# Kernel optimization log

Measured on AMD Instinct MI355X. Metric: run time of the kernel, lower is better.

Reference implementation:

```python
import jax, jax.numpy as jnp
import numpy as np

N_HEAD = 12

def setup_inputs() -> dict:
    key = jax.random.key(0)
    ks = jax.random.split(key, 5)
    C = 768
    B, T = 2, 2048
    s = 0.02
    x = jax.random.normal(ks[0], (B, T, C), dtype=jnp.float32)
    W_attn = jax.random.normal(ks[1], (C, 3 * C), dtype=jnp.float32) * s
    b_attn = jnp.zeros((3 * C,), dtype=jnp.float32)
    W_proj = jax.random.normal(ks[2], (C, C), dtype=jnp.float32) * s
    b_proj = jnp.zeros((C,), dtype=jnp.float32)
    return {"x": x, "W_attn": W_attn, "b_attn": b_attn, "W_proj": W_proj, "b_proj": b_proj}

def reference(x, W_attn, b_attn, W_proj, b_proj):
    B, T, C = x.shape
    H = N_HEAD
    hs = C // H
    qkv = x @ W_attn + b_attn                      # [B,T,3C]
    q, k, v = jnp.split(qkv, 3, axis=2)
    # [B,H,T,hs]
    q = q.reshape(B, T, H, hs).transpose(0, 2, 1, 3)
    k = k.reshape(B, T, H, hs).transpose(0, 2, 1, 3)
    v = v.reshape(B, T, H, hs).transpose(0, 2, 1, 3)
    scale = 1.0 / np.sqrt(hs).astype(np.float32)
    att = jnp.einsum('bhqd,bhkd->bhqk', q, k) * scale   # [B,H,T,T]
    causal = jnp.tril(jnp.ones((T, T), dtype=bool))
    att = jnp.where(causal, att, -jnp.inf)
    att = jax.nn.softmax(att, axis=-1)
    y = jnp.einsum('bhqk,bhkd->bhqd', att, v)            # [B,H,T,hs]
    y = y.transpose(0, 2, 1, 3).reshape(B, T, C)
    return y @ W_proj + b_proj
```

## Files before the change

### kernel.cpp

```cpp
#include <hip/hip_runtime.h>


#define BB 2
#define TT 2048
#define CC 768
#define C3 2304
#define HH 12
#define DD 64
#define MM 4096

typedef unsigned short u16;
typedef unsigned int u32;
typedef __attribute__((ext_vector_type(8))) u16 u16x8;
typedef __attribute__((ext_vector_type(8))) __bf16 bf16x8;
typedef __attribute__((ext_vector_type(4))) float f32x4;
typedef __attribute__((ext_vector_type(16))) float f32x16;

__device__ __forceinline__ float u2f(u16 u) {
    union { u32 i; float f; } c; c.i = ((u32)u) << 16; return c.f;
}
__device__ __forceinline__ u16 f2u(float f) {
    union { float f; u32 i; } c; c.f = f;
    u32 x = c.i;
    return (u16)((x + 0x7FFFu + ((x >> 16) & 1u)) >> 16);
}
__device__ __forceinline__ u16 f2b(float f) {
    __bf16 h = (__bf16)f; return __builtin_bit_cast(u16, h);
}
__device__ __forceinline__ bf16x8 ldsb8(const u16* p) {
    return __builtin_bit_cast(bf16x8, *(const u16x8*)p);
}
__device__ __forceinline__ f32x4 mfma16(bf16x8 a, bf16x8 b, f32x4 c) {
    return __builtin_amdgcn_mfma_f32_16x16x32_bf16(a, b, c, 0, 0, 0);
}
__device__ __forceinline__ f32x16 mfma32(bf16x8 a, bf16x8 b, f32x16 c) {
    return __builtin_amdgcn_mfma_f32_32x32x16_bf16(a, b, c, 0, 0, 0);
}
typedef __attribute__((address_space(1))) const u32 gu32;
typedef __attribute__((address_space(3))) u32 lu32;
__device__ __forceinline__ void gload16(const u16* gp, u16* lp) {
    __builtin_amdgcn_global_load_lds((gu32*)(const void*)gp, (lu32*)(void*)lp,
                                     16, 0, 0);
}
__device__ __forceinline__ void barrier_raw() {
    asm volatile("" ::: "memory");
    __builtin_amdgcn_s_barrier();
    asm volatile("" ::: "memory");
}

__global__ void detect_kernel(const u16* __restrict__ x, int* __restrict__ flag)
{
    __shared__ int found;
    if (threadIdx.x == 0) found = 0;
    __syncthreads();
    int local = 0;
    const u16x8* p = (const u16x8*)x + threadIdx.x;
    #pragma unroll
    for (int i = 0; i < 8; ++i) {
        const u16x8 v = p[(size_t)i * 256];
        #pragma unroll
        for (int j = 0; j < 8; ++j)
            if ((v[j] & 0x7F80u) == 0x7F80u) local = 1;
    }
    if (local) atomicOr(&found, 1);
    __syncthreads();
    if (threadIdx.x == 0) *flag = found ? 1 : 0;
}

__device__ void prep_w_body(const void* __restrict__ Wv, u16* __restrict__ Wt,
                            int K, int N, int bx, int by, int fm,
                            u16 (*Ts)[72])
{
    const int t = threadIdx.x;
    const int n0 = bx * 64, k0 = by * 64;
    const int r = t >> 2, c0 = (t & 3) << 4;

    if (fm) {
        const float* W = (const float*)Wv + (size_t)(k0 + r) * N + n0 + c0;
        #pragma unroll
        for (int i = 0; i < 16; i += 4) {
            const float4 v = *(const float4*)(W + i);
            Ts[c0 + i + 0][r] = f2u(v.x);
            Ts[c0 + i + 1][r] = f2u(v.y);
            Ts[c0 + i + 2][r] = f2u(v.z);
            Ts[c0 + i + 3][r] = f2u(v.w);
        }
    } else {
        const u16* W = (const u16*)Wv + (size_t)(k0 + r) * N + n0 + c0;
        const u16x8 a = *(const u16x8*)W;
        const u16x8 c = *(const u16x8*)(W + 8);
        #pragma unroll
        for (int i = 0; i < 8; ++i) { Ts[c0 + i][r] = a[i]; Ts[c0 + 8 + i][r] = c[i]; }
    }
    __syncthreads();
    u16* o = Wt + (size_t)(n0 + r) * K + k0 + c0;
    *(u16x8*)o = *(const u16x8*)&Ts[r][c0];
    *(u16x8*)(o + 8) = *(const u16x8*)&Ts[r][c0 + 8];
}

__global__ __launch_bounds__(256)
void fused_prep(const void* __restrict__ x, const void* __restrict__ Wa,
                const void* __restrict__ ba, const void* __restrict__ Wp,
                const void* __restrict__ bp,
                u16* __restrict__ xb, u16* __restrict__ WaT,
                u16* __restrict__ WpT, u16* __restrict__ bao,
                u16* __restrict__ bpo,
                const int* __restrict__ flag, int mode)
{
    __shared__ u16 Ts[64][72];
    const int fm = (mode >= 0) ? mode : *flag;
    const int blk = blockIdx.x;
    const int t = threadIdx.x;

    if (blk < 432) {
        prep_w_body(Wa, WaT, CC, C3, blk % 36, blk / 36, fm, Ts);
    } else if (blk < 576) {
        const int b2 = blk - 432;
        prep_w_body(Wp, WpT, CC, CC, b2 % 12, b2 / 12, fm, Ts);
    } else if (blk < 2112) {
        if (fm == 0) return;
        const size_t i = (size_t)(blk - 576) * 256 + t;
        const float* xp = (const float*)x + i * 8;
        u16x8 o;
        #pragma unroll
        for (int j = 0; j < 8; ++j) o[j] = f2u(xp[j]);
        *(u16x8*)(xb + i * 8) = o;
    } else {
        const int i = (blk - 2112) * 256 + t;
        if (i < C3) bao[i] = fm ? f2u(((const float*)ba)[i]) : ((const u16*)ba)[i];
        if (i < CC) bpo[i] = fm ? f2u(((const float*)bp)[i]) : ((const u16*)bp)[i];
    }
}

template <int FRM, int FRN>
__global__ __launch_bounds__(256)
void gemm_mfma(const u16* __restrict__ Adir, const u16* __restrict__ Acnv,
               const u16* __restrict__ Bt, const u16* __restrict__ bias,
               void* __restrict__ outv, int M, int N, int K,
               const int* __restrict__ flag, int mode, int om_sel)
{
    constexpr int TSM = 32 * FRM, TSN = 32 * FRN;
    constexpr int LPA = TSM / 64;
    constexpr int LPB = TSN / 64;

    __shared__ u16 As[2][TSM * 32];
    __shared__ u16 Bs[2][TSN * 32];

    const int fm = (mode >= 0) ? mode : *flag;
    const u16* A = fm ? Acnv : Adir;
    const int om = om_sel ? fm : 0;

    const int nwg = gridDim.x;
    const int lin = (blockIdx.x & 7) * (nwg >> 3) + (blockIdx.x >> 3);
    const int nx = N / TSN;
    const int m0 = (lin / nx) * TSM, n0 = (lin % nx) * TSN;

    const int t = threadIdx.x;
    const int lane = t & 63, wave = t >> 6;
    const int wm = wave >> 1, wn = wave & 1;
    const int l15 = lane & 15, h4 = lane >> 4;

    const int rsub = lane >> 2;
    const int cs = ((lane & 3) ^ ((lane >> 4) & 3)) * 8;
    const u16* Ab[LPA];
    const u16* Bb[LPB];
    #pragma unroll
    for (int j = 0; j < LPA; ++j)
        Ab[j] = A + (size_t)(m0 + wave * (16 * LPA) + j * 16 + rsub) * K + cs;
    #pragma unroll
    for (int j = 0; j < LPB; ++j)
        Bb[j] = Bt + (size_t)(n0 + wave * (16 * LPB) + j * 16 + rsub) * K + cs;

    f32x4 acc[FRM][FRN];
    #pragma unroll
    for (int i = 0; i < FRM; ++i)
        #pragma unroll
        for (int j = 0; j < FRN; ++j) acc[i][j] = (f32x4){0.f, 0.f, 0.f, 0.f};

    const int csr = (h4 ^ (l15 >> 2)) * 8;
    const int arow = wm * (TSM / 2) + l15;
    const int brow = wn * (TSN / 2) + l15;

    const int NT = K >> 5;
    #pragma unroll
    for (int j = 0; j < LPA; ++j)
        gload16(Ab[j], &As[0][(wave * LPA + j) * 512]);
    #pragma unroll
    for (int j = 0; j < LPB; ++j)
        gload16(Bb[j], &Bs[0][(wave * LPB + j) * 512]);

    for (int kt = 0; kt < NT; ++kt) {
        const int cur = kt & 1;
        if (kt + 1 < NT) {
            const int k0 = (kt + 1) << 5;
            const int nb = cur ^ 1;
            #pragma unroll
            for (int j = 0; j < LPA; ++j)
                gload16(Ab[j] + k0, &As[nb][(wave * LPA + j) * 512]);
            #pragma unroll
            for (int j = 0; j < LPB; ++j)
                gload16(Bb[j] + k0, &Bs[nb][(wave * LPB + j) * 512]);
            if constexpr (LPA + LPB == 4)
                asm volatile("s_waitcnt vmcnt(4)" ::: "memory");
            else if constexpr (LPA + LPB == 3)
                asm volatile("s_waitcnt vmcnt(3)" ::: "memory");
            else
                asm volatile("s_waitcnt vmcnt(2)" ::: "memory");
        } else {
            asm volatile("s_waitcnt vmcnt(0)" ::: "memory");
        }
        barrier_raw();

        bf16x8 af[FRM], bfr[FRN];
        #pragma unroll
        for (int f = 0; f < FRM; ++f)
            af[f] = ldsb8(&As[cur][(arow + f * 16) * 32 + csr]);
        #pragma unroll
        for (int f = 0; f < FRN; ++f)
            bfr[f] = ldsb8(&Bs[cur][(brow + f * 16) * 32 + csr]);
        #pragma unroll
        for (int i = 0; i < FRM; ++i)
            #pragma unroll
            for (int j = 0; j < FRN; ++j)
                acc[i][j] = mfma16(af[i], bfr[j], acc[i][j]);

        barrier_raw();
    }

    const int orow = m0 + wm * (TSM / 2) + h4 * 4;
    const int ocol = n0 + wn * (TSN / 2) + l15;
    if (om == 0) {
        u16* out = (u16*)outv;
        #pragma unroll
        for (int i = 0; i < FRM; ++i)
            #pragma unroll
            for (int j = 0; j < FRN; ++j) {
                const int col = ocol + j * 16;
                const float bv = u2f(bias[col]);
                #pragma unroll
                for (int r2 = 0; r2 < 4; ++r2)
                    out[(size_t)(orow + i * 16 + r2) * N + col] = f2b(acc[i][j][r2] + bv);
            }
    } else {
        float* out = (float*)outv;
        #pragma unroll
        for (int i = 0; i < FRM; ++i)
            #pragma unroll
            for (int j = 0; j < FRN; ++j) {
                const int col = ocol + j * 16;
                const float bv = u2f(bias[col]);
                #pragma unroll
                for (int r2 = 0; r2 < 4; ++r2)
                    out[(size_t)(orow + i * 16 + r2) * N + col] = acc[i][j][r2] + bv;
            }
    }
}

__global__ __launch_bounds__(256)
void attn_mfma(const u16* __restrict__ qkv, u16* __restrict__ yatt)
{
    __shared__ u16 Ks[2][64][72];
    __shared__ u16 Vt[2][64][72];

    const int bid = blockIdx.x;
    const int bin = bid & 255, slot = bid >> 8;
    const int g = bin >> 5, j = bin & 31;
    int qt;
    if (slot == 0)      qt = j;
    else if (slot == 1) qt = (j + 16) & 31;
    else                qt = (j < 16) ? (30 - 2 * j) : (63 - 2 * j);
    const int hb = slot * 8 + g;
    const int h = hb % HH, b = hb / HH;

    const int t = threadIdx.x;
    const int lane = t & 63, w = t >> 6;
    const int l31 = lane & 31, hl = lane >> 5;
    const int qh = w >> 1, kh = w & 1;
    const int q0 = qt * 64;
    const int qg = q0 + qh * 32 + l31;

    const int sr = t >> 2;
    const int sd = (t & 3) << 4;
    const int k5 = sr & 31;
    const int rr = (sr & 32) | (((k5 >> 2) & 1) << 4) | (((k5 >> 4) & 1) << 3)
                 | (((k5 >> 3) & 1) << 2) | (k5 & 3);
    const int vk = (t & 31) * 2;
    const int vd = (t >> 5) << 3;

    bf16x8 qf[4];
    {
        const u16* qp = qkv + ((size_t)(b * TT + qg)) * C3 + h * DD + hl * 8;
        #pragma unroll
        for (int t4 = 0; t4 < 4; ++t4) {
            const u16x8 v = *(const u16x8*)(qp + 16 * t4);
            #pragma unroll
            for (int i = 0; i < 8; ++i)
                qf[t4][i] = (__bf16)(u2f(v[i]) * 0.125f);
        }
    }

    float m_i = -1e4f, l_p = 0.f;
    f32x16 O0, O1;
    #pragma unroll
    for (int i = 0; i < 16; ++i) { O0[i] = 0.f; O1[i] = 0.f; }

    const u16* kB = qkv + ((size_t)(b * TT + sr)) * C3 + CC + h * DD + sd;
    const u16* vB = qkv + ((size_t)(b * TT + vk)) * C3 + 2 * CC + h * DD + vd;

    const int NT = qt + 1;

    u16x8 kr0 = *(const u16x8*)kB;
    u16x8 kr1 = *(const u16x8*)(kB + 8);
    u16x8 vr0 = *(const u16x8*)vB;
    u16x8 vr1 = *(const u16x8*)(vB + C3);
    *(u16x8*)&Ks[0][rr][sd]     = kr0;
    *(u16x8*)&Ks[0][rr][sd + 8] = kr1;
    #pragma unroll
    for (int i = 0; i < 8; ++i)
        *(u32*)&Vt[0][vd + i][vk] = (u32)vr0[i] | ((u32)vr1[i] << 16);
    if (NT > 1) {
        const u16* kp = kB + (size_t)64 * C3;
        const u16* vp = vB + (size_t)64 * C3;
        kr0 = *(const u16x8*)kp;
        kr1 = *(const u16x8*)(kp + 8);
        vr0 = *(const u16x8*)vp;
        vr1 = *(const u16x8*)(vp + C3);
    }
    __syncthreads();

    for (int kt = 0; kt < NT; ++kt) {
        const int cur = kt & 1;

        f32x16 s;
        #pragma unroll
        for (int i = 0; i < 16; ++i) s[i] = 0.f;
        __builtin_amdgcn_s_setprio(1);
        #pragma unroll
        for (int t4 = 0; t4 < 4; ++t4)
            s = mfma32(ldsb8(&Ks[cur][kh * 32 + l31][t4 * 16 + hl * 8]),
                       qf[t4], s);
        __builtin_amdgcn_s_setprio(0);

        if (kt + 1 < NT) {
            const int nb = cur ^ 1;
            *(u16x8*)&Ks[nb][rr][sd]     = kr0;
            *(u16x8*)&Ks[nb][rr][sd + 8] = kr1;
            #pragma unroll
            for (int i = 0; i < 8; ++i)
                *(u32*)&Vt[nb][vd + i][vk] = (u32)vr0[i] | ((u32)vr1[i] << 16);
            if (kt + 2 < NT) {
                const u16* kp = kB + (size_t)(kt + 2) * 64 * C3;
                const u16* vp = vB + (size_t)(kt + 2) * 64 * C3;
                kr0 = *(const u16x8*)kp;
                kr1 = *(const u16x8*)(kp + 8);
                vr0 = *(const u16x8*)vp;
                vr1 = *(const u16x8*)(vp + C3);
            }
        }

        if (kt == qt) {
            #pragma unroll
            for (int jj = 0; jj < 4; ++jj)
                #pragma unroll
                for (int e = 0; e < 4; ++e) {
                    const int kl = kh * 32 + ((jj & 1) << 4) + (hl << 3)
                                 + ((jj >> 1) << 2) + e;
                    if (kt * 64 + kl > qg) s[4 * jj + e] = -1e30f;
                }
        }

        float pm = s[0];
        #pragma unroll
        for (int i = 1; i < 16; ++i) pm = fmaxf(pm, s[i]);

        if (!__all(pm <= m_i + 8.f)) {
            const float pr = fmaxf(pm, __shfl_xor(pm, 32));
            const float mnew = fmaxf(m_i, pr);
            const float a_ = __expf(m_i - mnew);
            l_p *= a_;
            #pragma unroll
            for (int i = 0; i < 16; ++i) { O0[i] *= a_; O1[i] *= a_; }
            m_i = mnew;
        }

        bf16x8 p0, p1;
        float rs = 0.f;
        #pragma unroll
        for (int e = 0; e < 4; ++e) {
            const float a = __expf(s[e] - m_i);       rs += a; p0[e]     = (__bf16)a;
            const float c = __expf(s[8 + e] - m_i);   rs += c; p0[4 + e] = (__bf16)c;
            const float d = __expf(s[4 + e] - m_i);   rs += d; p1[e]     = (__bf16)d;
            const float g2 = __expf(s[12 + e] - m_i); rs += g2; p1[4 + e] = (__bf16)g2;
        }
        l_p += rs;

        __builtin_amdgcn_s_setprio(1);
        O0 = mfma32(ldsb8(&Vt[cur][l31][kh * 32 + hl * 8]), p0, O0);
        O0 = mfma32(ldsb8(&Vt[cur][l31][kh * 32 + 16 + hl * 8]), p1, O0);
        O1 = mfma32(ldsb8(&Vt[cur][32 + l31][kh * 32 + hl * 8]), p0, O1);
        O1 = mfma32(ldsb8(&Vt[cur][32 + l31][kh * 32 + 16 + hl * 8]), p1, O1);
        __builtin_amdgcn_s_setprio(0);

        __syncthreads();
    }

    const float lr = l_p + __shfl_xor(l_p, 32);

    float* scr = (float*)&Ks[0][0][0];
    const int sidx = (qh * 64 + lane) * 34;
    if (kh == 1) {
        scr[sidx] = m_i;
        scr[sidx + 1] = lr;
        #pragma unroll
        for (int i = 0; i < 16; ++i) {
            scr[sidx + 2 + i] = O0[i];
            scr[sidx + 18 + i] = O1[i];
        }
    }
    __syncthreads();
    if (kh == 0) {
        const float mB = scr[sidx], lB = scr[sidx + 1];
        const float mm = fmaxf(m_i, mB);
        const float a0 = __expf(m_i - mm), a1 = __expf(mB - mm);
        const float inv = 1.0f / (lr * a0 + lB * a1);
        u16* yp = yatt + ((size_t)(b * TT + qg)) * CC + h * DD;
        #pragma unroll
        for (int r = 0; r < 16; ++r) {
            const int drow = (r & 3) + 8 * (r >> 2) + 4 * hl;
            yp[drow]      = f2b((O0[r] * a0 + scr[sidx + 2 + r] * a1) * inv);
            yp[32 + drow] = f2b((O1[r] * a0 + scr[sidx + 18 + r] * a1) * inv);
        }
    }
}

extern "C" void kernel_launch(void* const* d_in, const int* in_sizes, int n_in,
                              void* d_out, int out_size, void* d_ws, size_t ws_size,
                              hipStream_t stream)
{
    (void)n_in; (void)out_size; (void)ws_size;

    const void* x      = d_in[0];
    const void* W_attn = d_in[1];
    const void* b_attn = d_in[2];
    const void* W_proj = d_in[3];
    const void* b_proj = d_in[4];

    u16* qkv  = (u16*)d_ws;
    u16* yatt = qkv + (size_t)MM * C3;
    u16* xb   = yatt;
    u16* WaT  = yatt + (size_t)MM * CC;
    u16* WpT  = WaT + (size_t)C3 * CC;
    u16* ba   = WpT + (size_t)CC * CC;
    u16* bp   = ba + C3;
    int* flag = (int*)(bp + CC);

    int mode = -1;
    if (in_sizes[0] == MM * CC * 4) mode = 1;
    else if (in_sizes[0] == MM * CC * 2) mode = 0;
    if (mode < 0) {
        detect_kernel<<<1, 256, 0, stream>>>((const u16*)x, flag);
    }

    fused_prep<<<2121, 256, 0, stream>>>(x, W_attn, b_attn, W_proj, b_proj,
                                         xb, WaT, WpT, ba, bp, flag, mode);

    gemm_mfma<4, 2><<<(MM / 128) * (C3 / 64), 256, 0, stream>>>(
        (const u16*)x, xb, WaT, ba, (void*)qkv, MM, C3, CC, flag, mode, 0);

    attn_mfma<<<dim3(TT / 64 * HH * BB, 1, 1), 256, 0, stream>>>(qkv, yatt);

    gemm_mfma<2, 2><<<(MM / 64) * (CC / 64), 256, 0, stream>>>(
        yatt, yatt, WpT, bp, d_out, MM, CC, CC, flag, mode, 1);
}
```

Baseline: 169.1 us.

## Use persistent attention blocks with atomic work queue, longest-first ordering

Replaces the static block-to-query-tile mapping in the attention kernel with persistent blocks that fetch work items from a global atomic counter. Items are ordered longest causal tile first, so the uneven causal workload is balanced dynamically across CUs. The counter is reset inside the prep kernel. Each item now costs an atomic plus an extra barrier, and 1024 blocks are launched for 768 items, so some blocks exit without doing any work.

```diff
diff --git a/kernel.cpp b/kernel.cpp
--- a/kernel.cpp
+++ b/kernel.cpp
@@ -8,6 +8,7 @@
 #define HH 12
 #define DD 64
 #define MM 4096
+#define NITEMS (32 * HH * BB)
 
 typedef unsigned short u16;
 typedef unsigned int u32;
@@ -105,7 +106,7 @@
                 u16* __restrict__ xb, u16* __restrict__ WaT,
                 u16* __restrict__ WpT, u16* __restrict__ bao,
                 u16* __restrict__ bpo,
-                const int* __restrict__ flag, int mode)
+                const int* __restrict__ flag, int mode, int* __restrict__ qcnt)
 {
     __shared__ u16 Ts[64][72];
     const int fm = (mode >= 0) ? mode : *flag;
@@ -126,6 +127,7 @@
         for (int j = 0; j < 8; ++j) o[j] = f2u(xp[j]);
         *(u16x8*)(xb + i * 8) = o;
     } else {
+        if (blk == 2112 && t == 0) *qcnt = 0;
         const int i = (blk - 2112) * 256 + t;
         if (i < C3) bao[i] = fm ? f2u(((const float*)ba)[i]) : ((const u16*)ba)[i];
         if (i < CC) bpo[i] = fm ? f2u(((const float*)bp)[i]) : ((const u16*)bp)[i];
@@ -257,27 +259,17 @@
 }
 
 __global__ __launch_bounds__(256)
-void attn_mfma(const u16* __restrict__ qkv, u16* __restrict__ yatt)
+void attn_mfma(const u16* __restrict__ qkv, u16* __restrict__ yatt,
+               int* __restrict__ qcnt)
 {
     __shared__ u16 Ks[2][64][72];
     __shared__ u16 Vt[2][64][72];
-
-    const int bid = blockIdx.x;
-    const int bin = bid & 255, slot = bid >> 8;
-    const int g = bin >> 5, j = bin & 31;
-    int qt;
-    if (slot == 0)      qt = j;
-    else if (slot == 1) qt = (j + 16) & 31;
-    else                qt = (j < 16) ? (30 - 2 * j) : (63 - 2 * j);
-    const int hb = slot * 8 + g;
-    const int h = hb % HH, b = hb / HH;
+    __shared__ int s_item;
 
     const int t = threadIdx.x;
     const int lane = t & 63, w = t >> 6;
     const int l31 = lane & 31, hl = lane >> 5;
     const int qh = w >> 1, kh = w & 1;
-    const int q0 = qt * 64;
-    const int qg = q0 + qh * 32 + l31;
 
     const int sr = t >> 2;
     const int sd = (t & 3) << 4;
@@ -287,149 +279,163 @@
     const int vk = (t & 31) * 2;
     const int vd = (t >> 5) << 3;
 
-    bf16x8 qf[4];
-    {
-        const u16* qp = qkv + ((size_t)(b * TT + qg)) * C3 + h * DD + hl * 8;
-        #pragma unroll
-        for (int t4 = 0; t4 < 4; ++t4) {
-            const u16x8 v = *(const u16x8*)(qp + 16 * t4);
-            #pragma unroll
-            for (int i = 0; i < 8; ++i)
-                qf[t4][i] = (__bf16)(u2f(v[i]) * 0.125f);
-        }
-    }
-
-    float m_i = -1e4f, l_p = 0.f;
-    f32x16 O0, O1;
-    #pragma unroll
-    for (int i = 0; i < 16; ++i) { O0[i] = 0.f; O1[i] = 0.f; }
-
-    const u16* kB = qkv + ((size_t)(b * TT + sr)) * C3 + CC + h * DD + sd;
-    const u16* vB = qkv + ((size_t)(b * TT + vk)) * C3 + 2 * CC + h * DD + vd;
-
-    const int NT = qt + 1;
-
-    u16x8 kr0 = *(const u16x8*)kB;
-    u16x8 kr1 = *(const u16x8*)(kB + 8);
-    u16x8 vr0 = *(const u16x8*)vB;
-    u16x8 vr1 = *(const u16x8*)(vB + C3);
-    *(u16x8*)&Ks[0][rr][sd]     = kr0;
-    *(u16x8*)&Ks[0][rr][sd + 8] = kr1;
-    #pragma unroll
-    for (int i = 0; i < 8; ++i)
-        *(u32*)&Vt[0][vd + i][vk] = (u32)vr0[i] | ((u32)vr1[i] << 16);
-    if (NT > 1) {
-        const u16* kp = kB + (size_t)64 * C3;
-        const u16* vp = vB + (size_t)64 * C3;
-        kr0 = *(const u16x8*)kp;
-        kr1 = *(const u16x8*)(kp + 8);
-        vr0 = *(const u16x8*)vp;
-        vr1 = *(const u16x8*)(vp + C3);
-    }
-    __syncthreads();
-
-    for (int kt = 0; kt < NT; ++kt) {
-        const int cur = kt & 1;
-
-        f32x16 s;
-        #pragma unroll
-        for (int i = 0; i < 16; ++i) s[i] = 0.f;
-        __builtin_amdgcn_s_setprio(1);
-        #pragma unroll
-        for (int t4 = 0; t4 < 4; ++t4)
-            s = mfma32(ldsb8(&Ks[cur][kh * 32 + l31][t4 * 16 + hl * 8]),
-                       qf[t4], s);
-        __builtin_amdgcn_s_setprio(0);
-
-        if (kt + 1 < NT) {
-            const int nb = cur ^ 1;
-            *(u16x8*)&Ks[nb][rr][sd]     = kr0;
-            *(u16x8*)&Ks[nb][rr][sd + 8] = kr1;
-            #pragma unroll
-            for (int i = 0; i < 8; ++i)
-                *(u32*)&Vt[nb][vd + i][vk] = (u32)vr0[i] | ((u32)vr1[i] << 16);
-            if (kt + 2 < NT) {
-                const u16* kp = kB + (size_t)(kt + 2) * 64 * C3;
-                const u16* vp = vB + (size_t)(kt + 2) * 64 * C3;
-                kr0 = *(const u16x8*)kp;
-                kr1 = *(const u16x8*)(kp + 8);
-                vr0 = *(const u16x8*)vp;
-                vr1 = *(const u16x8*)(vp + C3);
-            }
-        }
-
-        if (kt == qt) {
-            #pragma unroll
-            for (int jj = 0; jj < 4; ++jj)
-                #pragma unroll
-                for (int e = 0; e < 4; ++e) {
-                    const int kl = kh * 32 + ((jj & 1) << 4) + (hl << 3)
-                                 + ((jj >> 1) << 2) + e;
-                    if (kt * 64 + kl > qg) s[4 * jj + e] = -1e30f;
+    for (;;) {
+        if (t == 0) s_item = atomicAdd(qcnt, 1);
+        __syncthreads();
+        const int idx = s_item;
+        if (idx >= NITEMS) return;
+
+        const int qt = 31 - idx / (HH * BB);
+        const int hb = idx % (HH * BB);
+        const int h = hb % HH, b = hb / HH;
+        const int q0 = qt * 64;
+        const int qg = q0 + qh * 32 + l31;
+
+        bf16x8 qf[4];
+        {
+            const u16* qp = qkv + ((size_t)(b * TT + qg)) * C3 + h * DD + hl * 8;
+            #pragma unroll
+            for (int t4 = 0; t4 < 4; ++t4) {
+                const u16x8 v = *(const u16x8*)(qp + 16 * t4);
+                #pragma unroll
+                for (int i = 0; i < 8; ++i)
+                    qf[t4][i] = (__bf16)(u2f(v[i]) * 0.125f);
+            }
+        }
+
+        float m_i = -1e4f, l_p = 0.f;
+        f32x16 O0, O1;
+        #pragma unroll
+        for (int i = 0; i < 16; ++i) { O0[i] = 0.f; O1[i] = 0.f; }
+
+        const u16* kB = qkv + ((size_t)(b * TT + sr)) * C3 + CC + h * DD + sd;
+        const u16* vB = qkv + ((size_t)(b * TT + vk)) * C3 + 2 * CC + h * DD + vd;
+
+        const int NT = qt + 1;
+
+        u16x8 kr0 = *(const u16x8*)kB;
+        u16x8 kr1 = *(const u16x8*)(kB + 8);
+        u16x8 vr0 = *(const u16x8*)vB;
+        u16x8 vr1 = *(const u16x8*)(vB + C3);
+        *(u16x8*)&Ks[0][rr][sd]     = kr0;
+        *(u16x8*)&Ks[0][rr][sd + 8] = kr1;
+        #pragma unroll
+        for (int i = 0; i < 8; ++i)
+            *(u32*)&Vt[0][vd + i][vk] = (u32)vr0[i] | ((u32)vr1[i] << 16);
+        if (NT > 1) {
+            const u16* kp = kB + (size_t)64 * C3;
+            const u16* vp = vB + (size_t)64 * C3;
+            kr0 = *(const u16x8*)kp;
+            kr1 = *(const u16x8*)(kp + 8);
+            vr0 = *(const u16x8*)vp;
+            vr1 = *(const u16x8*)(vp + C3);
+        }
+        __syncthreads();
+
+        for (int kt = 0; kt < NT; ++kt) {
+            const int cur = kt & 1;
+
+            f32x16 s;
+            #pragma unroll
+            for (int i = 0; i < 16; ++i) s[i] = 0.f;
+            __builtin_amdgcn_s_setprio(1);
+            #pragma unroll
+            for (int t4 = 0; t4 < 4; ++t4)
+                s = mfma32(ldsb8(&Ks[cur][kh * 32 + l31][t4 * 16 + hl * 8]),
+                           qf[t4], s);
+            __builtin_amdgcn_s_setprio(0);
+
+            if (kt + 1 < NT) {
+                const int nb = cur ^ 1;
+                *(u16x8*)&Ks[nb][rr][sd]     = kr0;
+                *(u16x8*)&Ks[nb][rr][sd + 8] = kr1;
+                #pragma unroll
+                for (int i = 0; i < 8; ++i)
+                    *(u32*)&Vt[nb][vd + i][vk] = (u32)vr0[i] | ((u32)vr1[i] << 16);
+                if (kt + 2 < NT) {
+                    const u16* kp = kB + (size_t)(kt + 2) * 64 * C3;
+                    const u16* vp = vB + (size_t)(kt + 2) * 64 * C3;
+                    kr0 = *(const u16x8*)kp;
+                    kr1 = *(const u16x8*)(kp + 8);
+                    vr0 = *(const u16x8*)vp;
+                    vr1 = *(const u16x8*)(vp + C3);
                 }
-        }
-
-        float pm = s[0];
-        #pragma unroll
-        for (int i = 1; i < 16; ++i) pm = fmaxf(pm, s[i]);
-
-        if (!__all(pm <= m_i + 8.f)) {
-            const float pr = fmaxf(pm, __shfl_xor(pm, 32));
-            const float mnew = fmaxf(m_i, pr);
-            const float a_ = __expf(m_i - mnew);
-            l_p *= a_;
-            #pragma unroll
-            for (int i = 0; i < 16; ++i) { O0[i] *= a_; O1[i] *= a_; }
-            m_i = mnew;
-        }
-
-        bf16x8 p0, p1;
-        float rs = 0.f;
-        #pragma unroll
-        for (int e = 0; e < 4; ++e) {
-            const float a = __expf(s[e] - m_i);       rs += a; p0[e]     = (__bf16)a;
-            const float c = __expf(s[8 + e] - m_i);   rs += c; p0[4 + e] = (__bf16)c;
-            const float d = __expf(s[4 + e] - m_i);   rs += d; p1[e]     = (__bf16)d;
-            const float g2 = __expf(s[12 + e] - m_i); rs += g2; p1[4 + e] = (__bf16)g2;
-        }
-        l_p += rs;
-
-        __builtin_amdgcn_s_setprio(1);
-        O0 = mfma32(ldsb8(&Vt[cur][l31][kh * 32 + hl * 8]), p0, O0);
-        O0 = mfma32(ldsb8(&Vt[cur][l31][kh * 32 + 16 + hl * 8]), p1, O0);
-        O1 = mfma32(ldsb8(&Vt[cur][32 + l31][kh * 32 + hl * 8]), p0, O1);
-        O1 = mfma32(ldsb8(&Vt[cur][32 + l31][kh * 32 + 16 + hl * 8]), p1, O1);
-        __builtin_amdgcn_s_setprio(0);
-
+            }
+
+            if (kt == qt) {
+                #pragma unroll
+                for (int jj = 0; jj < 4; ++jj)
+                    #pragma unroll
+                    for (int e = 0; e < 4; ++e) {
+                        const int kl = kh * 32 + ((jj & 1) << 4) + (hl << 3)
+                                     + ((jj >> 1) << 2) + e;
+                        if (kt * 64 + kl > qg) s[4 * jj + e] = -1e30f;
+                    }
+            }
+
+            float pm = s[0];
+            #pragma unroll
+            for (int i = 1; i < 16; ++i) pm = fmaxf(pm, s[i]);
+
+            if (!__all(pm <= m_i + 8.f)) {
+                const float pr = fmaxf(pm, __shfl_xor(pm, 32));
+                const float mnew = fmaxf(m_i, pr);
+                const float a_ = __expf(m_i - mnew);
+                l_p *= a_;
+                #pragma unroll
+                for (int i = 0; i < 16; ++i) { O0[i] *= a_; O1[i] *= a_; }
+                m_i = mnew;
+            }
+
+            bf16x8 p0, p1;
+            float rs = 0.f;
+            #pragma unroll
+            for (int e = 0; e < 4; ++e) {
+                const float a = __expf(s[e] - m_i);       rs += a; p0[e]     = (__bf16)a;
+                const float c = __expf(s[8 + e] - m_i);   rs += c; p0[4 + e] = (__bf16)c;
+                const float d = __expf(s[4 + e] - m_i);   rs += d; p1[e]     = (__bf16)d;
+                const float g2 = __expf(s[12 + e] - m_i); rs += g2; p1[4 + e] = (__bf16)g2;
+            }
+            l_p += rs;
+
+            __builtin_amdgcn_s_setprio(1);
+            O0 = mfma32(ldsb8(&Vt[cur][l31][kh * 32 + hl * 8]), p0, O0);
+            O0 = mfma32(ldsb8(&Vt[cur][l31][kh * 32 + 16 + hl * 8]), p1, O0);
+            O1 = mfma32(ldsb8(&Vt[cur][32 + l31][kh * 32 + hl * 8]), p0, O1);
+            O1 = mfma32(ldsb8(&Vt[cur][32 + l31][kh * 32 + 16 + hl * 8]), p1, O1);
+            __builtin_amdgcn_s_setprio(0);
+
+            __syncthreads();
+        }
+
+        const float lr = l_p + __shfl_xor(l_p, 32);
+
+        float* scr = (float*)&Ks[0][0][0];
+        const int sidx = (qh * 64 + lane) * 34;
+        if (kh == 1) {
+            scr[sidx] = m_i;
+            scr[sidx + 1] = lr;
+            #pragma unroll
+            for (int i = 0; i < 16; ++i) {
+                scr[sidx + 2 + i] = O0[i];
+                scr[sidx + 18 + i] = O1[i];
+            }
+        }
         __syncthreads();
-    }
-
-    const float lr = l_p + __shfl_xor(l_p, 32);
-
-    float* scr = (float*)&Ks[0][0][0];
-    const int sidx = (qh * 64 + lane) * 34;
-    if (kh == 1) {
-        scr[sidx] = m_i;
-        scr[sidx + 1] = lr;
-        #pragma unroll
-        for (int i = 0; i < 16; ++i) {
-            scr[sidx + 2 + i] = O0[i];
-            scr[sidx + 18 + i] = O1[i];
-        }
-    }
-    __syncthreads();
-    if (kh == 0) {
-        const float mB = scr[sidx], lB = scr[sidx + 1];
-        const float mm = fmaxf(m_i, mB);
-        const float a0 = __expf(m_i - mm), a1 = __expf(mB - mm);
-        const float inv = 1.0f / (lr * a0 + lB * a1);
-        u16* yp = yatt + ((size_t)(b * TT + qg)) * CC + h * DD;
-        #pragma unroll
-        for (int r = 0; r < 16; ++r) {
-            const int drow = (r & 3) + 8 * (r >> 2) + 4 * hl;
-            yp[drow]      = f2b((O0[r] * a0 + scr[sidx + 2 + r] * a1) * inv);
-            yp[32 + drow] = f2b((O1[r] * a0 + scr[sidx + 18 + r] * a1) * inv);
-        }
+        if (kh == 0) {
+            const float mB = scr[sidx], lB = scr[sidx + 1];
+            const float mm = fmaxf(m_i, mB);
+            const float a0 = __expf(m_i - mm), a1 = __expf(mB - mm);
+            const float inv = 1.0f / (lr * a0 + lB * a1);
+            u16* yp = yatt + ((size_t)(b * TT + qg)) * CC + h * DD;
+            #pragma unroll
+            for (int r = 0; r < 16; ++r) {
+                const int drow = (r & 3) + 8 * (r >> 2) + 4 * hl;
+                yp[drow]      = f2b((O0[r] * a0 + scr[sidx + 2 + r] * a1) * inv);
+                yp[32 + drow] = f2b((O1[r] * a0 + scr[sidx + 18 + r] * a1) * inv);
+            }
+        }
+        __syncthreads();
     }
 }
 
@@ -453,6 +459,7 @@
     u16* ba   = WpT + (size_t)CC * CC;
     u16* bp   = ba + C3;
     int* flag = (int*)(bp + CC);
+    int* qcnt = flag + 1;
 
     int mode = -1;
     if (in_sizes[0] == MM * CC * 4) mode = 1;
@@ -462,12 +469,12 @@
     }
 
     fused_prep<<<2121, 256, 0, stream>>>(x, W_attn, b_attn, W_proj, b_proj,
-                                         xb, WaT, WpT, ba, bp, flag, mode);
+                                         xb, WaT, WpT, ba, bp, flag, mode, qcnt);
 
     gemm_mfma<4, 2><<<(MM / 128) * (C3 / 64), 256, 0, stream>>>(
         (const u16*)x, xb, WaT, ba, (void*)qkv, MM, C3, CC, flag, mode, 0);
 
-    attn_mfma<<<dim3(TT / 64 * HH * BB, 1, 1), 256, 0, stream>>>(qkv, yatt);
+    attn_mfma<<<dim3(1024, 1, 1), 256, 0, stream>>>(qkv, yatt, qcnt);
 
     gemm_mfma<2, 2><<<(MM / 64) * (CC / 64), 256, 0, stream>>>(
         yatt, yatt, WpT, bp, d_out, MM, CC, CC, flag, mode, 1);
```

Result: no change. 172.3 us (+1.8%).
